# Kernel tuning notes

Measured on AMD Instinct MI355X. Metric: run time of the kernel, lower is better.

## Reference

```python
import math
import jax, jax.numpy as jnp
import numpy as np

EMBED_DIM = 1024
NUM_HEADS = 16
HEAD_DIM = EMBED_DIM // NUM_HEADS
ROTARY_DIM = HEAD_DIM  # default: rotary_dim = head_dim
BASE = 10000.0


def _rope_cos_sin(seq_len, d, dtype=jnp.float32):
    # theta: [d/2], positions: [S]
    theta = 1.0 / (BASE ** (jnp.arange(0, d, 2, dtype=jnp.float32) / d))
    pos = jnp.arange(seq_len, dtype=jnp.float32)
    idx_theta = pos[:, None] * theta[None, :]          # [S, d/2]
    idx_theta2 = jnp.concatenate([idx_theta, idx_theta], axis=-1)  # [S, d]
    return jnp.cos(idx_theta2).astype(dtype), jnp.sin(idx_theta2).astype(dtype)


def _apply_rope(x):
    # x: [B, H, S, head_dim]; rotate first ROTARY_DIM features
    S = x.shape[-2]
    cos, sin = _rope_cos_sin(S, ROTARY_DIM, x.dtype)   # [S, ROTARY_DIM]
    x_rope, x_pass = x[..., :ROTARY_DIM], x[..., ROTARY_DIM:]
    d2 = ROTARY_DIM // 2
    neg_half = jnp.concatenate([-x_rope[..., d2:], x_rope[..., :d2]], axis=-1)
    x_rope = x_rope * cos + neg_half * sin
    return jnp.concatenate([x_rope, x_pass], axis=-1)


def setup_inputs() -> dict:
    key = jax.random.key(0)
    ks = jax.random.split(key, 9)
    B, S, E = 4, 2048, EMBED_DIM
    scale = 1.0 / math.sqrt(E)
    inp = {
        "x": jax.random.normal(ks[0], (B, S, E), dtype=jnp.float32),
        "attn_mask": jnp.ones((B, S), dtype=jnp.int32),
        "Wq": jax.random.normal(ks[1], (E, E), dtype=jnp.float32) * scale,
        "bq": jnp.zeros((E,), dtype=jnp.float32),
        "Wk": jax.random.normal(ks[2], (E, E), dtype=jnp.float32) * scale,
        "bk": jnp.zeros((E,), dtype=jnp.float32),
        "Wv": jax.random.normal(ks[3], (E, E), dtype=jnp.float32) * scale,
        "bv": jnp.zeros((E,), dtype=jnp.float32),
        "Wo": jax.random.normal(ks[4], (E, E), dtype=jnp.float32) * scale,
        "bo": jnp.zeros((E,), dtype=jnp.float32),
    }
    return inp


def reference(x, attn_mask, Wq, bq, Wk, bk, Wv, bv, Wo, bo):
    B, S, E = x.shape
    H, D = NUM_HEADS, HEAD_DIM

    def proj(W, b):
        # [B,S,E] -> [B,H,S,D]
        y = jnp.einsum('bse,ef->bsf', x, W) + b
        return y.reshape(B, S, H, D).transpose(0, 2, 1, 3)

    q = _apply_rope(proj(Wq, bq))
    k = _apply_rope(proj(Wk, bk))
    v = proj(Wv, bv)

    scores = jnp.einsum('bhsd,bhtd->bhst', q, k) / math.sqrt(D)  # [B,H,S,S]
    mask = attn_mask[:, None, None, :]  # [B,1,1,S]
    scores = jnp.where(mask == 0, jnp.float32(-1e9).astype(scores.dtype), scores)
    attn = jax.nn.softmax(scores, axis=-1)
    out = jnp.einsum('bhst,bhtd->bhsd', attn, v)  # [B,H,S,D]
    out = out.transpose(0, 2, 1, 3).reshape(B, S, E)
    return jnp.einsum('bse,ef->bsf', out, Wo) + bo
```

## Files before the change

### kernel.cpp

```cpp
#include <hip/hip_runtime.h>
#include <math.h>

typedef __attribute__((ext_vector_type(8))) short short8;
typedef __attribute__((ext_vector_type(4))) float f32x4;
typedef __attribute__((ext_vector_type(4))) unsigned short us4;
typedef __attribute__((ext_vector_type(4))) unsigned int u32x4;
typedef __attribute__((ext_vector_type(4))) int i32x4;
typedef unsigned short u16;
typedef unsigned int u32;

#define LOG2E 1.4426950408889634f

static __device__ __forceinline__ u16 f2bf(float f){
  u32 u = __builtin_bit_cast(u32, f);
  u = (u + 0x7FFFu + ((u >> 16) & 1u)) >> 16;
  return (u16)u;
}

static __device__ __forceinline__ void gload16(const void* g, void* l){
  __builtin_amdgcn_global_load_lds((const __attribute__((address_space(1))) void*)g,
                                   (__attribute__((address_space(3))) void*)l,
                                   16, 0, 0);
}

static __device__ __forceinline__ f32x4 mfma16(short8 a, short8 b, f32x4 c){
  return __builtin_amdgcn_mfma_f32_16x16x32_bf16(a, b, c, 0, 0, 0);
}

__global__ void rope_tab_k(float* __restrict__ cosT, float* __restrict__ sinT){
  int idx = blockIdx.x * 256 + threadIdx.x;
  int s = idx >> 5, i = idx & 31;
  double th = pow(10000.0, -((double)(2 * i)) / 64.0);
  float ang = (float)s * (float)th;
  cosT[idx] = (float)cos((double)ang);
  sinT[idx] = (float)sin((double)ang);
}

__global__ void cvt_x_k(const float* __restrict__ x, u16* __restrict__ xb, int n){
  int i = (blockIdx.x * 256 + threadIdx.x) * 4;
  if (i >= n) return;
  f32x4 v = *(const f32x4*)(x + i);
  us4 o; o[0]=f2bf(v[0]); o[1]=f2bf(v[1]); o[2]=f2bf(v[2]); o[3]=f2bf(v[3]);
  *(us4*)(xb + i) = o;
}

__global__ void wt_cvt_k(const float* __restrict__ W0, const float* __restrict__ W1,
                         const float* __restrict__ W2, const float* __restrict__ W3,
                         u16* __restrict__ out){
  __shared__ float t[32][33];
  const float* W = (blockIdx.z == 0) ? W0 : (blockIdx.z == 1) ? W1 : (blockIdx.z == 2) ? W2 : W3;
  u16* O = out + (size_t)blockIdx.z * 1024 * 1024;
  int tx = threadIdx.x, ty = threadIdx.y;
  int kb = blockIdx.y * 32, nb = blockIdx.x * 32;
  #pragma unroll
  for (int i = 0; i < 4; i++)
    t[ty + i*8][tx] = W[(size_t)(kb + ty + i*8) * 1024 + nb + tx];
  __syncthreads();
  #pragma unroll
  for (int i = 0; i < 4; i++)
    O[(size_t)(nb + ty + i*8) * 1024 + kb + tx] = f2bf(t[tx][ty + i*8]);
}

__global__ __launch_bounds__(256, 2)
void qkv_gemm_k(const u16* __restrict__ A, const u16* __restrict__ WT,
                const float* __restrict__ bq, const float* __restrict__ bk,
                const float* __restrict__ bv,
                const float* __restrict__ cosT, const float* __restrict__ sinT,
                u16* __restrict__ Qr, u16* __restrict__ Kr, u16* __restrict__ Vt)
{
  __shared__ __align__(16) u16 Al[128][64];
  __shared__ __align__(16) u16 Bl[128][64];
  const int mode = blockIdx.y >> 3;
  const int cy   = blockIdx.y & 7;
  const u16* BT = WT + (size_t)mode * 1024 * 1024;
  const float* bias = (mode == 0) ? bq : (mode == 1) ? bk : bv;
  u16* outB = (mode == 0) ? Qr : (mode == 1) ? Kr : Vt;

  const int tid = threadIdx.x;
  const int w = tid >> 6, lane = tid & 63, g = lane >> 4, c = lane & 15;
  const int wr = w >> 1, wc = w & 1;
  const int R0 = blockIdx.x * 128, C0 = cy * 128;

  f32x4 acc[4][4];
  const f32x4 vz = {0.f, 0.f, 0.f, 0.f};
  #pragma unroll
  for (int mi = 0; mi < 4; mi++)
    #pragma unroll
    for (int ni = 0; ni < 4; ni++) acc[mi][ni] = vz;

  const u16* gA[4]; const u16* gB[4]; u16* lA[4]; u16* lB[4];
  #pragma unroll
  for (int i = 0; i < 4; i++){
    int I = w * 4 + i;
    int rr = I * 8 + (lane >> 3), kk = (lane & 7) * 8;
    gA[i] = A  + (size_t)(R0 + rr) * 1024 + kk;
    gB[i] = BT + (size_t)(C0 + rr) * 1024 + kk;
    lA[i] = &Al[I * 8][0];
    lB[i] = &Bl[I * 8][0];
  }

  for (int t = 0; t < 16; ++t){
    const int k0 = t * 64;
    #pragma unroll
    for (int i = 0; i < 4; i++){
      gload16(gA[i] + k0, lA[i]);
      gload16(gB[i] + k0, lB[i]);
    }
    __syncthreads();
    #pragma unroll
    for (int ki = 0; ki < 2; ++ki){
      short8 af[4], bfr[4];
      #pragma unroll
      for (int mi = 0; mi < 4; mi++) af[mi]  = *(const short8*)&Al[wr*64 + mi*16 + c][ki*32 + g*8];
      #pragma unroll
      for (int ni = 0; ni < 4; ni++) bfr[ni] = *(const short8*)&Bl[wc*64 + ni*16 + c][ki*32 + g*8];
      #pragma unroll
      for (int mi = 0; mi < 4; mi++)
        #pragma unroll
        for (int ni = 0; ni < 4; ni++)
          acc[mi][ni] = mfma16(af[mi], bfr[ni], acc[mi][ni]);
    }
    __syncthreads();
  }

  if (mode == 2){
    int h = cy * 2 + wc;
    #pragma unroll
    for (int ni = 0; ni < 4; ni++){
      int col = C0 + wc*64 + ni*16 + c;
      int d = ni*16 + c;
      float bvv = bias[col];
      #pragma unroll
      for (int mi = 0; mi < 4; mi++){
        int row0 = R0 + wr*64 + mi*16 + g*4;
        int b = row0 >> 11, s0 = row0 & 2047;
        us4 pk;
        #pragma unroll
        for (int r = 0; r < 4; r++) pk[r] = f2bf(acc[mi][ni][r] + bvv);
        *(us4*)&outB[((size_t)(b*16 + h)*64 + d)*2048 + s0] = pk;
      }
    }
  } else {
    int h = cy * 2 + wc;
    const float qs = (mode == 0) ? 0.125f : 1.0f;
    float bvv[4];
    #pragma unroll
    for (int ni = 0; ni < 4; ni++) bvv[ni] = bias[C0 + wc*64 + ni*16 + c];
    #pragma unroll
    for (int mi = 0; mi < 4; mi++){
      int row0 = R0 + wr*64 + mi*16 + g*4;
      int b = row0 >> 11;
      #pragma unroll
      for (int r = 0; r < 4; r++){
        int s = (row0 + r) & 2047;
        float v0 = acc[mi][0][r] + bvv[0];
        float v1 = acc[mi][1][r] + bvv[1];
        float v2 = acc[mi][2][r] + bvv[2];
        float v3 = acc[mi][3][r] + bvv[3];
        float ca = cosT[s*32 + c],      sa = sinT[s*32 + c];
        float cb = cosT[s*32 + 16 + c], sb = sinT[s*32 + 16 + c];
        float o0 = (v0*ca - v2*sa) * qs, o2 = (v2*ca + v0*sa) * qs;
        float o1 = (v1*cb - v3*sb) * qs, o3 = (v3*cb + v1*sb) * qs;
        size_t base = ((size_t)(b*16 + h)*2048 + s)*64;
        outB[base +  0 + c] = f2bf(o0);
        outB[base + 16 + c] = f2bf(o1);
        outB[base + 32 + c] = f2bf(o2);
        outB[base + 48 + c] = f2bf(o3);
      }
    }
  }
}

__global__ __launch_bounds__(256, 2)
void out_gemm_k(const u16* __restrict__ A, const u16* __restrict__ BT,
                const float* __restrict__ bias, float* __restrict__ outF)
{
  __shared__ __align__(16) u16 Al[128][64];
  __shared__ __align__(16) u16 Bl[128][64];
  const int tid = threadIdx.x;
  const int w = tid >> 6, lane = tid & 63, g = lane >> 4, c = lane & 15;
  const int wr = w >> 1, wc = w & 1;
  const int R0 = blockIdx.x * 128, C0 = blockIdx.y * 128;

  f32x4 acc[4][4];
  const f32x4 vz = {0.f, 0.f, 0.f, 0.f};
  #pragma unroll
  for (int mi = 0; mi < 4; mi++)
    #pragma unroll
    for (int ni = 0; ni < 4; ni++) acc[mi][ni] = vz;

  const u16* gA[4]; const u16* gB[4]; u16* lA[4]; u16* lB[4];
  #pragma unroll
  for (int i = 0; i < 4; i++){
    int I = w * 4 + i;
    int rr = I * 8 + (lane >> 3), kk = (lane & 7) * 8;
    gA[i] = A  + (size_t)(R0 + rr) * 1024 + kk;
    gB[i] = BT + (size_t)(C0 + rr) * 1024 + kk;
    lA[i] = &Al[I * 8][0];
    lB[i] = &Bl[I * 8][0];
  }

  for (int t = 0; t < 16; ++t){
    const int k0 = t * 64;
    #pragma unroll
    for (int i = 0; i < 4; i++){
      gload16(gA[i] + k0, lA[i]);
      gload16(gB[i] + k0, lB[i]);
    }
    __syncthreads();
    #pragma unroll
    for (int ki = 0; ki < 2; ++ki){
      short8 af[4], bfr[4];
      #pragma unroll
      for (int mi = 0; mi < 4; mi++) af[mi]  = *(const short8*)&Al[wr*64 + mi*16 + c][ki*32 + g*8];
      #pragma unroll
      for (int ni = 0; ni < 4; ni++) bfr[ni] = *(const short8*)&Bl[wc*64 + ni*16 + c][ki*32 + g*8];
      #pragma unroll
      for (int mi = 0; mi < 4; mi++)
        #pragma unroll
        for (int ni = 0; ni < 4; ni++)
          acc[mi][ni] = mfma16(af[mi], bfr[ni], acc[mi][ni]);
    }
    __syncthreads();
  }

  #pragma unroll
  for (int mi = 0; mi < 4; mi++){
    #pragma unroll
    for (int ni = 0; ni < 4; ni++){
      int col = C0 + wc*64 + ni*16 + c;
      float bvv = bias[col];
      int row0 = R0 + wr*64 + mi*16 + g*4;
      #pragma unroll
      for (int r = 0; r < 4; r++)
        outF[(size_t)(row0 + r) * 1024 + col] = acc[mi][ni][r] + bvv;
    }
  }
}

__global__ __launch_bounds__(256, 4)
void attn_fwd_k(const u16* __restrict__ Q, const u16* __restrict__ K, const u16* __restrict__ V,
                const int* __restrict__ msk, u16* __restrict__ AO)
{
  __shared__ __align__(16) u16 Kl[2][64][64];
  __shared__ __align__(16) u16 Vl[2][64][64];
  __shared__ int Ml[2048];
  const int tid = threadIdx.x;
  const int w = tid >> 6, lane = tid & 63, g = lane >> 4, c = lane & 15;

  const int lin = blockIdx.y * 16 + blockIdx.x;
  const int v_  = (lin & 7) * 128 + (lin >> 3);
  const int bh = v_ >> 4, b = bh >> 4, h = bh & 15;
  const int qw = (v_ & 15) * 128 + w * 32;

  const int l3 = lane >> 3, l7 = lane & 7;
  const int scol = (l7 ^ l3) * 8;
  const u16* gK[2]; const u16* gV[2];
  #pragma unroll
  for (int i = 0; i < 2; i++){
    int s = (w*2 + i)*8 + l3;
    int ps = (s & 0x20) | ((s & 0x10) >> 2) | ((s & 0x0C) << 1) | (s & 3);
    gK[i] = K + ((size_t)bh*2048 + ps)*64 + scol;
    gV[i] = V + ((size_t)bh*64 + s)*2048 + scol;
  }

  {
    const int* ms = msk + b*2048 + w*512 + lane*4;
    gload16(ms,       &Ml[w*512]);
    gload16(ms + 256, &Ml[w*512 + 256]);
  }
  #pragma unroll
  for (int i = 0; i < 2; i++){
    gload16(gK[i], &Kl[0][(w*2+i)*8][0]);
    gload16(gV[i], &Vl[0][(w*2+i)*8][0]);
  }

  short8 qb[2][2];
  #pragma unroll
  for (int mq = 0; mq < 2; mq++)
    #pragma unroll
    for (int ki = 0; ki < 2; ki++)
      qb[mq][ki] = *(const short8*)&Q[((size_t)bh*2048 + qw + mq*16 + c)*64 + ki*32 + g*8];

  f32x4 oacc[2][4];
  float mrun[2], lrun[2];
  const f32x4 vz = {0.f, 0.f, 0.f, 0.f};
  #pragma unroll
  for (int mq = 0; mq < 2; mq++){
    #pragma unroll
    for (int nd = 0; nd < 4; nd++) oacc[mq][nd] = vz;
    mrun[mq] = -1e30f; lrun[mq] = 0.f;
  }

  const int cs0 = (g*8) ^ ((c & 7) << 3);
  const int cs1 = (32 + g*8) ^ ((c & 7) << 3);

  for (int t = 0; t < 32; ++t){
    {
      const size_t ko = (size_t)(t+1) * 64 * 64;
      const size_t vo = (size_t)(t+1) * 64;
      #pragma unroll
      for (int i = 0; i < 2; i++){
        gload16(gK[i] + ko, &Kl[(t+1)&1][(w*2+i)*8][0]);
        gload16(gV[i] + vo, &Vl[(t+1)&1][(w*2+i)*8][0]);
      }
    }
    asm volatile("s_waitcnt vmcnt(4)" ::: "memory");
    __builtin_amdgcn_s_barrier();
    asm volatile("" ::: "memory");

    const u16* Kb = &Kl[t&1][0][0];
    const u16* Vb = &Vl[t&1][0][0];
    const int t0 = t * 64;

    f32x4 sacc[4][2];
    #pragma unroll
    for (int nt = 0; nt < 4; nt++){ sacc[nt][0] = vz; sacc[nt][1] = vz; }
    #pragma unroll
    for (int ki = 0; ki < 2; ki++){
      const int cs = ki ? cs1 : cs0;
      short8 ka[4];
      #pragma unroll
      for (int nt = 0; nt < 4; nt++) ka[nt] = *(const short8*)&Kb[(nt*16 + c)*64 + cs];
      #pragma unroll
      for (int nt = 0; nt < 4; nt++)
        #pragma unroll
        for (int mq = 0; mq < 2; mq++)
          sacc[nt][mq] = mfma16(ka[nt], qb[mq][ki], sacc[nt][mq]);
    }

    i32x4 mv[4];
    #pragma unroll
    for (int nt = 0; nt < 4; nt++)
      mv[nt] = *(const i32x4*)&Ml[t0 + 32*(nt>>1) + 8*g + 4*(nt&1)];
    int ma = (mv[0][0] & mv[0][1]) & (mv[0][2] & mv[0][3]);
    ma &= (mv[1][0] & mv[1][1]) & (mv[1][2] & mv[1][3]);
    ma &= (mv[2][0] & mv[2][1]) & (mv[2][2] & mv[2][3]);
    ma &= (mv[3][0] & mv[3][1]) & (mv[3][2] & mv[3][3]);
    if (!__all(ma != 0)){
      #pragma unroll
      for (int nt = 0; nt < 4; nt++)
        #pragma unroll
        for (int r = 0; r < 4; r++){
          if (mv[nt][r] == 0){ sacc[nt][0][r] = -1e9f; sacc[nt][1][r] = -1e9f; }
        }
    }

    float al[2];
    short8 pa[2][2];
    #pragma unroll
    for (int mq = 0; mq < 2; mq++){
      float m16 = sacc[0][mq][0];
      #pragma unroll
      for (int nt = 0; nt < 4; nt++)
        #pragma unroll
        for (int r = 0; r < 4; r++)
          m16 = fmaxf(m16, sacc[nt][mq][r]);
      m16 = fmaxf(m16, __shfl_xor(m16, 16, 64));
      m16 = fmaxf(m16, __shfl_xor(m16, 32, 64));
      float mn = fmaxf(mrun[mq], m16);
      al[mq] = exp2f((mrun[mq] - mn) * LOG2E);
      mrun[mq] = mn;
      const float nm = -mn * LOG2E;
      u32 prB[4][4];
      float sum = 0.f;
      #pragma unroll
      for (int nt = 0; nt < 4; nt++)
        #pragma unroll
        for (int r = 0; r < 4; r++){
          float p = exp2f(fmaf(sacc[nt][mq][r], LOG2E, nm));
          u32 pb = (u32)f2bf(p) << 16;
          prB[nt][r] = pb;
          sum += __builtin_bit_cast(float, pb);
        }
      sum += __shfl_xor(sum, 16, 64);
      sum += __shfl_xor(sum, 32, 64);
      lrun[mq] = lrun[mq] * al[mq] + sum;
      #pragma unroll
      for (int ki = 0; ki < 2; ki++){
        u32x4 pk;
        pk[0] = (prB[2*ki  ][0] >> 16) | prB[2*ki  ][1];
        pk[1] = (prB[2*ki  ][2] >> 16) | prB[2*ki  ][3];
        pk[2] = (prB[2*ki+1][0] >> 16) | prB[2*ki+1][1];
        pk[3] = (prB[2*ki+1][2] >> 16) | prB[2*ki+1][3];
        pa[mq][ki] = __builtin_bit_cast(short8, pk);
      }
    }

    #pragma unroll
    for (int mq = 0; mq < 2; mq++){
      float a0 = __shfl(al[mq], g*4 + 0, 64);
      float a1 = __shfl(al[mq], g*4 + 1, 64);
      float a2 = __shfl(al[mq], g*4 + 2, 64);
      float a3 = __shfl(al[mq], g*4 + 3, 64);
      #pragma unroll
      for (int nd = 0; nd < 4; nd++){
        oacc[mq][nd][0] *= a0; oacc[mq][nd][1] *= a1;
        oacc[mq][nd][2] *= a2; oacc[mq][nd][3] *= a3;
      }
    }

    #pragma unroll
    for (int ki = 0; ki < 2; ki++){
      const int cs = ki ? cs1 : cs0;
      short8 va[4];
      #pragma unroll
      for (int nd = 0; nd < 4; nd++) va[nd] = *(const short8*)&Vb[(nd*16 + c)*64 + cs];
      #pragma unroll
      for (int mq = 0; mq < 2; mq++)
        #pragma unroll
        for (int nd = 0; nd < 4; nd++)
          oacc[mq][nd] = mfma16(pa[mq][ki], va[nd], oacc[mq][nd]);
    }

    asm volatile("" ::: "memory");
    __builtin_amdgcn_s_barrier();
    asm volatile("" ::: "memory");
  }

  #pragma unroll
  for (int mq = 0; mq < 2; mq++){
    #pragma unroll
    for (int r = 0; r < 4; r++){
      float li = __shfl(lrun[mq], g*4 + r, 64);
      float inv = 1.0f / li;
      int q = qw + mq*16 + g*4 + r;
      size_t base = ((size_t)b*2048 + q)*1024 + h*64;
      #pragma unroll
      for (int nd = 0; nd < 4; nd++)
        AO[base + nd*16 + c] = f2bf(oacc[mq][nd][r] * inv);
    }
  }
}

extern "C" void kernel_launch(void* const* d_in, const int* in_sizes, int n_in,
                              void* d_out, int out_size, void* d_ws, size_t ws_size,
                              hipStream_t stream)
{
  const float* x  = (const float*)d_in[0];
  const int* mask = (const int*)d_in[1];
  const float* Wq = (const float*)d_in[2];
  const float* bq = (const float*)d_in[3];
  const float* Wk = (const float*)d_in[4];
  const float* bk = (const float*)d_in[5];
  const float* Wv = (const float*)d_in[6];
  const float* bv = (const float*)d_in[7];
  const float* Wo = (const float*)d_in[8];
  const float* bo = (const float*)d_in[9];
  float* out = (float*)d_out;
  (void)in_sizes; (void)n_in; (void)out_size; (void)ws_size;

  char* ws = (char*)d_ws;
  size_t off = 0;
  auto alloc = [&](size_t bytes){ void* p = ws + off; off += (bytes + 255) & ~(size_t)255; return p; };
  u16* xb    = (u16*)alloc((size_t)8192 * 1024 * 2);
  u16* WT    = (u16*)alloc((size_t)4 * 1024 * 1024 * 2);
  float* cosT = (float*)alloc((size_t)2048 * 32 * 4);
  float* sinT = (float*)alloc((size_t)2048 * 32 * 4);
  u16* Qr    = (u16*)alloc((size_t)8192 * 1024 * 2);
  u16* Kr    = (u16*)alloc((size_t)8192 * 1024 * 2);
  u16* Vt    = (u16*)alloc((size_t)8192 * 1024 * 2);
  u16* AO    = (u16*)alloc((size_t)8192 * 1024 * 2);

  rope_tab_k<<<dim3(256), dim3(256), 0, stream>>>(cosT, sinT);
  cvt_x_k<<<dim3(8192), dim3(256), 0, stream>>>(x, xb, 8192 * 1024);
  wt_cvt_k<<<dim3(32, 32, 4), dim3(32, 8), 0, stream>>>(Wq, Wk, Wv, Wo, WT);

  qkv_gemm_k<<<dim3(64, 24), dim3(256), 0, stream>>>(xb, WT, bq, bk, bv, cosT, sinT, Qr, Kr, Vt);

  attn_fwd_k<<<dim3(16, 64), dim3(256), 0, stream>>>(Qr, Kr, Vt, mask, AO);

  out_gemm_k<<<dim3(64, 8), dim3(256), 0, stream>>>(AO, WT + 3*1024*1024, bo, out);
}
```

Baseline: 264.2 us.

## Add lazy softmax rescaling, byte-packed mask, and perm-based bf16 packing in attention

Rescales the running max and the output accumulator only when a new row maximum exceeds the old one by more than a threshold, skipping the per-tile exp and shuffle rescale in the common case. The mask is staged as bytes in LDS via register loads instead of int32 async loads. The bf16 packing of probabilities now uses v_perm, and the row sum is taken from the fp32 probabilities in a tree. Risks include reduced numerical headroom from the lazy max (probabilities up to 2^11.5) and a small sum mismatch versus the bf16-rounded P.

```diff
diff --git a/kernel.cpp b/kernel.cpp
--- a/kernel.cpp
+++ b/kernel.cpp
@@ -244,7 +244,7 @@
 {
   __shared__ __align__(16) u16 Kl[2][64][64];
   __shared__ __align__(16) u16 Vl[2][64][64];
-  __shared__ int Ml[2048];
+  __shared__ __align__(8) unsigned char Ml[2048];
   const int tid = threadIdx.x;
   const int w = tid >> 6, lane = tid & 63, g = lane >> 4, c = lane & 15;
 
@@ -252,6 +252,24 @@
   const int v_  = (lin & 7) * 128 + (lin >> 3);
   const int bh = v_ >> 4, b = bh >> 4, h = bh & 15;
   const int qw = (v_ & 15) * 128 + w * 32;
+
+  {
+    const int* mp = msk + b*2048 + tid*8;
+    i32x4 a = *(const i32x4*)mp;
+    i32x4 d2 = *(const i32x4*)(mp + 4);
+    u32 lo = (a[0]  ? 1u : 0u) | (a[1]  ? 0x100u : 0u) | (a[2]  ? 0x10000u : 0u) | (a[3]  ? 0x1000000u : 0u);
+    u32 hi = (d2[0] ? 1u : 0u) | (d2[1] ? 0x100u : 0u) | (d2[2] ? 0x10000u : 0u) | (d2[3] ? 0x1000000u : 0u);
+    *(u32*)&Ml[tid*8]     = lo;
+    *(u32*)&Ml[tid*8 + 4] = hi;
+  }
+  asm volatile("s_waitcnt lgkmcnt(0)" ::: "memory");
+
+  short8 qb[2][2];
+  #pragma unroll
+  for (int mq = 0; mq < 2; mq++)
+    #pragma unroll
+    for (int ki = 0; ki < 2; ki++)
+      qb[mq][ki] = *(const short8*)&Q[((size_t)bh*2048 + qw + mq*16 + c)*64 + ki*32 + g*8];
 
   const int l3 = lane >> 3, l7 = lane & 7;
   const int scol = (l7 ^ l3) * 8;
@@ -263,24 +281,11 @@
     gK[i] = K + ((size_t)bh*2048 + ps)*64 + scol;
     gV[i] = V + ((size_t)bh*64 + s)*2048 + scol;
   }
-
-  {
-    const int* ms = msk + b*2048 + w*512 + lane*4;
-    gload16(ms,       &Ml[w*512]);
-    gload16(ms + 256, &Ml[w*512 + 256]);
-  }
   #pragma unroll
   for (int i = 0; i < 2; i++){
     gload16(gK[i], &Kl[0][(w*2+i)*8][0]);
     gload16(gV[i], &Vl[0][(w*2+i)*8][0]);
   }
-
-  short8 qb[2][2];
-  #pragma unroll
-  for (int mq = 0; mq < 2; mq++)
-    #pragma unroll
-    for (int ki = 0; ki < 2; ki++)
-      qb[mq][ki] = *(const short8*)&Q[((size_t)bh*2048 + qw + mq*16 + c)*64 + ki*32 + g*8];
 
   f32x4 oacc[2][4];
   float mrun[2], lrun[2];
@@ -329,75 +334,89 @@
           sacc[nt][mq] = mfma16(ka[nt], qb[mq][ki], sacc[nt][mq]);
     }
 
-    i32x4 mv[4];
-    #pragma unroll
-    for (int nt = 0; nt < 4; nt++)
-      mv[nt] = *(const i32x4*)&Ml[t0 + 32*(nt>>1) + 8*g + 4*(nt&1)];
-    int ma = (mv[0][0] & mv[0][1]) & (mv[0][2] & mv[0][3]);
-    ma &= (mv[1][0] & mv[1][1]) & (mv[1][2] & mv[1][3]);
-    ma &= (mv[2][0] & mv[2][1]) & (mv[2][2] & mv[2][3]);
-    ma &= (mv[3][0] & mv[3][1]) & (mv[3][2] & mv[3][3]);
-    if (!__all(ma != 0)){
+    {
+      const u32 mw0 = *(const u32*)&Ml[t0 + 8*g];
+      const u32 mw1 = *(const u32*)&Ml[t0 + 8*g + 4];
+      const u32 mw2 = *(const u32*)&Ml[t0 + 32 + 8*g];
+      const u32 mw3 = *(const u32*)&Ml[t0 + 32 + 8*g + 4];
+      if (!__all((mw0 & mw1 & mw2 & mw3) == 0x01010101u)){
+        const u32 mw[4] = {mw0, mw1, mw2, mw3};
+        #pragma unroll
+        for (int nt = 0; nt < 4; nt++)
+          #pragma unroll
+          for (int r = 0; r < 4; r++)
+            if (((mw[nt] >> (8*r)) & 0xFFu) == 0){ sacc[nt][0][r] = -1e9f; sacc[nt][1][r] = -1e9f; }
+      }
+    }
+
+    float pm[2];
+    #pragma unroll
+    for (int mq = 0; mq < 2; mq++){
+      float a0 = fmaxf(fmaxf(sacc[0][mq][0], sacc[0][mq][1]), fmaxf(sacc[0][mq][2], sacc[0][mq][3]));
+      float a1 = fmaxf(fmaxf(sacc[1][mq][0], sacc[1][mq][1]), fmaxf(sacc[1][mq][2], sacc[1][mq][3]));
+      float a2 = fmaxf(fmaxf(sacc[2][mq][0], sacc[2][mq][1]), fmaxf(sacc[2][mq][2], sacc[2][mq][3]));
+      float a3 = fmaxf(fmaxf(sacc[3][mq][0], sacc[3][mq][1]), fmaxf(sacc[3][mq][2], sacc[3][mq][3]));
+      float mm = fmaxf(fmaxf(a0, a1), fmaxf(a2, a3));
+      mm = fmaxf(mm, __shfl_xor(mm, 16, 64));
+      mm = fmaxf(mm, __shfl_xor(mm, 32, 64));
+      pm[mq] = mm;
+    }
+
+    if (__any((pm[0] > mrun[0] + 8.f) | (pm[1] > mrun[1] + 8.f))){
+      float al[2];
+      #pragma unroll
+      for (int mq = 0; mq < 2; mq++){
+        float mn = fmaxf(mrun[mq], pm[mq]);
+        al[mq] = exp2f((mrun[mq] - mn) * LOG2E);
+        mrun[mq] = mn;
+        lrun[mq] *= al[mq];
+      }
+      #pragma unroll
+      for (int mq = 0; mq < 2; mq++){
+        float b0 = __shfl(al[mq], g*4 + 0, 64);
+        float b1 = __shfl(al[mq], g*4 + 1, 64);
+        float b2 = __shfl(al[mq], g*4 + 2, 64);
+        float b3 = __shfl(al[mq], g*4 + 3, 64);
+        #pragma unroll
+        for (int nd = 0; nd < 4; nd++){
+          oacc[mq][nd][0] *= b0; oacc[mq][nd][1] *= b1;
+          oacc[mq][nd][2] *= b2; oacc[mq][nd][3] *= b3;
+        }
+      }
+    }
+
+    short8 pa[2][2];
+    #pragma unroll
+    for (int mq = 0; mq < 2; mq++){
+      const float nm = -mrun[mq] * LOG2E;
+      float p[16]; u32 rb[16];
       #pragma unroll
       for (int nt = 0; nt < 4; nt++)
         #pragma unroll
         for (int r = 0; r < 4; r++){
-          if (mv[nt][r] == 0){ sacc[nt][0][r] = -1e9f; sacc[nt][1][r] = -1e9f; }
+          float pp = exp2f(fmaf(sacc[nt][mq][r], LOG2E, nm));
+          p[nt*4 + r] = pp;
+          u32 u = __builtin_bit_cast(u32, pp);
+          rb[nt*4 + r] = u + 0x7FFFu + ((u >> 16) & 1u);
         }
-    }
-
-    float al[2];
-    short8 pa[2][2];
-    #pragma unroll
-    for (int mq = 0; mq < 2; mq++){
-      float m16 = sacc[0][mq][0];
-      #pragma unroll
-      for (int nt = 0; nt < 4; nt++)
-        #pragma unroll
-        for (int r = 0; r < 4; r++)
-          m16 = fmaxf(m16, sacc[nt][mq][r]);
-      m16 = fmaxf(m16, __shfl_xor(m16, 16, 64));
-      m16 = fmaxf(m16, __shfl_xor(m16, 32, 64));
-      float mn = fmaxf(mrun[mq], m16);
-      al[mq] = exp2f((mrun[mq] - mn) * LOG2E);
-      mrun[mq] = mn;
-      const float nm = -mn * LOG2E;
-      u32 prB[4][4];
-      float sum = 0.f;
-      #pragma unroll
-      for (int nt = 0; nt < 4; nt++)
-        #pragma unroll
-        for (int r = 0; r < 4; r++){
-          float p = exp2f(fmaf(sacc[nt][mq][r], LOG2E, nm));
-          u32 pb = (u32)f2bf(p) << 16;
-          prB[nt][r] = pb;
-          sum += __builtin_bit_cast(float, pb);
-        }
+      float s0 = (p[0] + p[1]) + (p[2] + p[3]);
+      float s1 = (p[4] + p[5]) + (p[6] + p[7]);
+      float s2 = (p[8] + p[9]) + (p[10] + p[11]);
+      float s3 = (p[12] + p[13]) + (p[14] + p[15]);
+      float sum = (s0 + s1) + (s2 + s3);
       sum += __shfl_xor(sum, 16, 64);
       sum += __shfl_xor(sum, 32, 64);
-      lrun[mq] = lrun[mq] * al[mq] + sum;
-      #pragma unroll
-      for (int ki = 0; ki < 2; ki++){
-        u32x4 pk;
-        pk[0] = (prB[2*ki  ][0] >> 16) | prB[2*ki  ][1];
-        pk[1] = (prB[2*ki  ][2] >> 16) | prB[2*ki  ][3];
-        pk[2] = (prB[2*ki+1][0] >> 16) | prB[2*ki+1][1];
-        pk[3] = (prB[2*ki+1][2] >> 16) | prB[2*ki+1][3];
-        pa[mq][ki] = __builtin_bit_cast(short8, pk);
-      }
-    }
-
-    #pragma unroll
-    for (int mq = 0; mq < 2; mq++){
-      float a0 = __shfl(al[mq], g*4 + 0, 64);
-      float a1 = __shfl(al[mq], g*4 + 1, 64);
-      float a2 = __shfl(al[mq], g*4 + 2, 64);
-      float a3 = __shfl(al[mq], g*4 + 3, 64);
-      #pragma unroll
-      for (int nd = 0; nd < 4; nd++){
-        oacc[mq][nd][0] *= a0; oacc[mq][nd][1] *= a1;
-        oacc[mq][nd][2] *= a2; oacc[mq][nd][3] *= a3;
-      }
+      lrun[mq] += sum;
+      u32x4 q0 = { __builtin_amdgcn_perm(rb[1],  rb[0],  0x07060302u),
+                   __builtin_amdgcn_perm(rb[3],  rb[2],  0x07060302u),
+                   __builtin_amdgcn_perm(rb[5],  rb[4],  0x07060302u),
+                   __builtin_amdgcn_perm(rb[7],  rb[6],  0x07060302u) };
+      u32x4 q1 = { __builtin_amdgcn_perm(rb[9],  rb[8],  0x07060302u),
+                   __builtin_amdgcn_perm(rb[11], rb[10], 0x07060302u),
+                   __builtin_amdgcn_perm(rb[13], rb[12], 0x07060302u),
+                   __builtin_amdgcn_perm(rb[15], rb[14], 0x07060302u) };
+      pa[mq][0] = __builtin_bit_cast(short8, q0);
+      pa[mq][1] = __builtin_bit_cast(short8, q1);
     }
 
     #pragma unroll
```

Result: no change. 262.7 us (-0.6%).
